# Kernel tuning notes

Hardware: AMD Instinct MI355X
Metric: run time of the kernel (lower is better)

## Reference

```python
import jax, jax.numpy as jnp
import numpy as np

HIDDEN = 1024
NUM_HEADS = 16
HEAD_DIM = HIDDEN // NUM_HEADS
EPS = 1e-12


def _layernorm(x, g, b):
    mu = jnp.mean(x, axis=-1, keepdims=True)
    var = jnp.var(x, axis=-1, keepdims=True)
    return (x - mu) * jax.lax.rsqrt(var + EPS) * g + b


def _attention(q, k, v, mask, Wd, bd, ln_g, ln_b):
    # q: [B,T,H], k/v: [B,S,H], mask: [B,1,1,S] additive
    B, T, _ = q.shape
    S = k.shape[1]
    qh = q.reshape(B, T, NUM_HEADS, HEAD_DIM).transpose(0, 2, 1, 3)  # [B,h,T,d]
    kh = k.reshape(B, S, NUM_HEADS, HEAD_DIM).transpose(0, 2, 1, 3)
    vh = v.reshape(B, S, NUM_HEADS, HEAD_DIM).transpose(0, 2, 1, 3)
    scores = jnp.einsum('bhtd,bhsd->bhts', qh, kh) / jnp.sqrt(jnp.float32(HEAD_DIM))
    if mask is not None:
        scores = scores + mask
    probs = jax.nn.softmax(scores, axis=-1)  # dropout = identity in eval
    ctx = jnp.einsum('bhts,bhsd->bthd', probs, vh)  # [B,T,h,d]
    # torch: w = dense.weight.t().view(h, d, H); einsum('bfnd,ndh->bfh')
    w = Wd.T.reshape(NUM_HEADS, HEAD_DIM, HIDDEN)
    proj = jnp.einsum('bthd,hdH->btH', ctx, w) + bd
    # residual is the (projected) query tensor q, per source
    return _layernorm(q + proj, ln_g, ln_b)


def setup_inputs() -> dict:
    key = jax.random.key(0)
    ks = jax.random.split(key, 12)
    s = 0.02
    B, S, T = 4, 1024, 1024
    return {
        'encoder_states': jax.random.normal(ks[0], (B, S, HIDDEN), jnp.float32),
        'decoder_inputs': jax.random.normal(ks[1], (B, T, HIDDEN), jnp.float32),
        'src_attention_mask': jnp.zeros((B, 1, 1, S), jnp.float32),
        'tgt_attention_mask': jnp.zeros((B, 1, 1, T), jnp.float32),
        'Wq': jax.random.normal(ks[2], (HIDDEN, HIDDEN), jnp.float32) * s,
        'bq': jnp.zeros((HIDDEN,), jnp.float32),
        'Wk': jax.random.normal(ks[3], (HIDDEN, HIDDEN), jnp.float32) * s,
        'bk': jnp.zeros((HIDDEN,), jnp.float32),
        'Wv': jax.random.normal(ks[4], (HIDDEN, HIDDEN), jnp.float32) * s,
        'bv': jnp.zeros((HIDDEN,), jnp.float32),
        'Wd': jax.random.normal(ks[5], (HIDDEN, HIDDEN), jnp.float32) * s,
        'bd': jnp.zeros((HIDDEN,), jnp.float32),
        'ln_g': jnp.ones((HIDDEN,), jnp.float32),
        'ln_b': jnp.zeros((HIDDEN,), jnp.float32),
    }


def reference(encoder_states, decoder_inputs, src_attention_mask, tgt_attention_mask,
              Wq, bq, Wk, bk, Wv, bv, Wd, bd, ln_g, ln_b):
    # projections (torch Linear: x @ W.T + b)
    q1 = decoder_inputs @ Wq.T + bq
    k1 = decoder_inputs @ Wk.T + bk
    v1 = decoder_inputs @ Wv.T + bv
    ek = encoder_states @ Wk.T + bk
    ev = encoder_states @ Wv.T + bv
    # self-attention over decoder states
    self_out = _attention(q1, k1, v1, tgt_attention_mask, Wd, bd, ln_g, ln_b)
    # cross-attention: query = self_out directly (no extra projection, per source)
    out = _attention(self_out, ek, ev, src_attention_mask, Wd, bd, ln_g, ln_b)
    return out
```

## Files before the change

kernel.cpp:

```cpp
#include <hip/hip_runtime.h>
#include <stdint.h>


#define B_   4
#define T_   1024
#define S_   1024
#define H_   1024
#define LOG2E 1.44269504088896340736f
#define SCALE_K (0.125f * LOG2E)

typedef __attribute__((ext_vector_type(8)))  __bf16       bf16x8;
typedef __attribute__((ext_vector_type(4)))  float        f32x4;
typedef __attribute__((ext_vector_type(16))) float        f32x16;
typedef __attribute__((ext_vector_type(4)))  unsigned int uint4v;

static __device__ __forceinline__ float bf2f(unsigned int u) {
    return __builtin_bit_cast(float, u << 16);
}
static __device__ __forceinline__ unsigned short f2bf(float f) {
    unsigned int x = __builtin_bit_cast(unsigned int, f);
    return (unsigned short)((x + 0x7fffu + ((x >> 16) & 1u)) >> 16);
}
static __device__ __forceinline__ unsigned int cvt_pk_bf16(float lo, float hi) {
    unsigned int r;
    asm("v_cvt_pk_bf16_f32 %0, %1, %2" : "=v"(r) : "v"(lo), "v"(hi));
    return r;
}
static __device__ __forceinline__ void perm32swap(unsigned int& a, unsigned int& b) {
    asm("v_permlane32_swap_b32 %0, %1" : "+v"(a), "+v"(b));
}
static __device__ __forceinline__ f32x4 mfma16(bf16x8 a, bf16x8 b, f32x4 c) {
    return __builtin_amdgcn_mfma_f32_16x16x32_bf16(a, b, c, 0, 0, 0);
}
static __device__ __forceinline__ f32x16 mfma32(bf16x8 a, bf16x8 b, f32x16 c) {
    return __builtin_amdgcn_mfma_f32_32x32x16_bf16(a, b, c, 0, 0, 0);
}

typedef const __attribute__((address_space(1))) void gv_t;
typedef __attribute__((address_space(3))) void lv_t;
static __device__ __forceinline__ void g2lds16(const void* g, void* l) {
    __builtin_amdgcn_global_load_lds((gv_t*)(size_t)g, (lv_t*)(unsigned int)(size_t)l, 16, 0, 0);
}

struct CvtArgs {
    const float* src[6];
    unsigned short* dst[6];
    float scale[6];
    int n4[6];
};
__global__ __launch_bounds__(256)
void cvt_multi(CvtArgs a) {
    const int k = blockIdx.y;
    const int i = blockIdx.x * 256 + threadIdx.x;
    if (i >= a.n4[k]) return;
    const float s = a.scale[k];
    float4 v = ((const float4*)a.src[k])[i];
    uint2 o;
    o.x = (unsigned)f2bf(v.x * s) | ((unsigned)f2bf(v.y * s) << 16);
    o.y = (unsigned)f2bf(v.z * s) | ((unsigned)f2bf(v.w * s) << 16);
    ((uint2*)a.dst[k])[i] = o;
}

struct GemmJob {
    const unsigned short* A[5];
    const unsigned short* W[5];
    const float* bias[5];
    float bs[5];
    unsigned short* O[5];
    unsigned short* OT[5];
    int koff[5];
    int klen[5];
};
__global__ __launch_bounds__(256, 4)
void gemm_bf16(GemmJob job)
{
    __shared__ char smem[32768];
    char* As = smem;
    char* Bs = smem + 16384;
    const int tid = threadIdx.x;
    const int lane = tid & 63;
    const int w = tid >> 6;
    const int c = lane & 15, g = lane >> 4;
    const int wm = (w >> 1) * 64, wn = (w & 1) * 64;
    const int m0 = blockIdx.x * 128;
    const int set = blockIdx.y >> 3;
    const int n0 = (blockIdx.y & 7) * 128;
    const unsigned short* A    = job.A[set];
    const unsigned short* W    = job.W[set];
    const float* bias          = job.bias[set];
    const float bscale         = job.bs[set];
    unsigned short* O          = job.O[set];
    unsigned short* OT         = job.OT[set];
    const int koff             = job.koff[set];
    const int kend             = koff + job.klen[set];

    f32x4 acc[4][4];
#pragma unroll
    for (int i = 0; i < 4; i++)
#pragma unroll
        for (int j = 0; j < 4; j++) acc[i][j] = (f32x4){0.f, 0.f, 0.f, 0.f};

    const int srow = w * 32 + (lane >> 3);
    const int swzc = ((lane & 7) ^ (lane >> 3)) * 8;
    const unsigned short* gA = A + (size_t)(m0 + srow) * 1024 + swzc;
    const unsigned short* gB = W + (size_t)(n0 + srow) * 1024 + swzc;
    char* lA = As + w * 4096;
    char* lB = Bs + w * 4096;

    for (int kk = koff; kk < kend; kk += 64) {
#pragma unroll
        for (int q = 0; q < 4; q++) {
            g2lds16(gA + kk + q*8192, lA + q*1024);
            g2lds16(gB + kk + q*8192, lB + q*1024);
        }
        __syncthreads();
#pragma unroll
        for (int ksub = 0; ksub < 2; ksub++) {
            bf16x8 af[4], bfr[4];
#pragma unroll
            for (int t = 0; t < 4; t++) {
                const int ra = wm + t*16 + c;
                const int rb = wn + t*16 + c;
                const int so = ((ksub*4 + g) ^ (c & 7)) << 4;
                af[t]  = *(const bf16x8*)(As + ra*128 + so);
                bfr[t] = *(const bf16x8*)(Bs + rb*128 + so);
            }
#pragma unroll
            for (int i = 0; i < 4; i++)
#pragma unroll
                for (int j = 0; j < 4; j++)
                    acc[i][j] = mfma16(af[i], bfr[j], acc[i][j]);
        }
        __syncthreads();
    }

    float bvv[4];
#pragma unroll
    for (int j = 0; j < 4; j++) bvv[j] = bias[n0 + wn + j*16 + c] * bscale;

    if (OT == nullptr) {
        char* eb = smem + w * 4096;
#pragma unroll
        for (int p = 0; p < 2; p++) {
#pragma unroll
            for (int ii = 0; ii < 2; ii++) {
                const int i = p*2 + ii;
#pragma unroll
                for (int j = 0; j < 4; j++)
#pragma unroll
                    for (int r = 0; r < 4; r++)
                        *(unsigned short*)(eb + (ii*16 + g*4 + r)*128 + (c + j*16)*2)
                            = f2bf(acc[i][j][r] + bvv[j]);
            }
            asm volatile("s_waitcnt lgkmcnt(0)" ::: "memory");
#pragma unroll
            for (int it = 0; it < 4; it++) {
                const int lrow = it*8 + (lane >> 3);
                uint4 vv = *(const uint4*)(eb + lrow*128 + (lane & 7)*16);
                *(uint4*)(O + (size_t)(m0 + wm + p*32 + lrow)*1024 + n0 + wn + (lane & 7)*8) = vv;
            }
            if (p == 0) asm volatile("s_waitcnt lgkmcnt(0)" ::: "memory");
        }
    } else {
        char* ebT = smem + w * 8192;
        const int n_glob = n0 + wn + lane;
        const int hh = n_glob >> 6, dd = n_glob & 63;
        const int bidx = m0 >> 10;
        unsigned short* vout0 = OT + ((size_t)((bidx*16 + hh)*64 + dd))*S_ + (m0 & 1023) + wm;
#pragma unroll
        for (int p = 0; p < 2; p++) {
#pragma unroll
            for (int ii = 0; ii < 2; ii++) {
                const int i = p*2 + ii;
#pragma unroll
                for (int j = 0; j < 4; j++) {
                    uint2 pw;
                    pw.x = (unsigned)f2bf(acc[i][j][0] + bvv[j]) |
                           ((unsigned)f2bf(acc[i][j][1] + bvv[j]) << 16);
                    pw.y = (unsigned)f2bf(acc[i][j][2] + bvv[j]) |
                           ((unsigned)f2bf(acc[i][j][3] + bvv[j]) << 16);
                    *(uint2*)(ebT + (j*16 + c)*72 + (ii*16 + g*4)*2) = pw;
                }
            }
            asm volatile("s_waitcnt lgkmcnt(0)" ::: "memory");
            unsigned short* vout = vout0 + p*32;
#pragma unroll
            for (int q = 0; q < 4; q++) {
                uint2 r0 = *(const uint2*)(ebT + lane*72 + (q*2    )*8);
                uint2 r1 = *(const uint2*)(ebT + lane*72 + (q*2 + 1)*8);
                uint4 vv; vv.x = r0.x; vv.y = r0.y; vv.z = r1.x; vv.w = r1.y;
                *(uint4*)(vout + q*8) = vv;
            }
            if (p == 0) asm volatile("s_waitcnt lgkmcnt(0)" ::: "memory");
        }
    }
}

__global__ __launch_bounds__(256, 4)
void attn_fused2(const unsigned short* __restrict__ Q,
                 const unsigned short* __restrict__ Kx,
                 const unsigned short* __restrict__ VT,
                 const float* __restrict__ mask,
                 unsigned short* __restrict__ Octx)
{
    __shared__ char smem[32768 + 4096 + 512 + 16];
    float* mb   = (float*)(smem + 32768);
    float* lbuf = (float*)(smem + 32768 + 4096);
    int* flag   = (int*)(smem + 32768 + 4096 + 512);

    const int tid = threadIdx.x;
    const int lane = tid & 63, w = tid >> 6;
    const int qc = lane & 31, hi = lane >> 5;
    const int bh = blockIdx.x, b = bh >> 4, h = bh & 15;
    const int q0 = blockIdx.y * 128 + w * 32;

    const int r0 = tid >> 3, sg = tid & 7;
    const unsigned short* gK0 = Kx + (size_t)(b*S_ + r0)*H_  + h*64 + sg*8;
    const unsigned short* gK1 = gK0 + (size_t)32*H_;
    const unsigned short* gV0 = VT + (size_t)(bh*64 + r0)*S_ + sg*8;
    const unsigned short* gV1 = gV0 + (size_t)32*S_;
    const int woff = r0*128 + ((sg*16) ^ ((r0 & 7) << 4));

    const unsigned short* qptr = Q + (size_t)(b*T_ + q0 + qc)*H_ + h*64 + hi*8;
    bf16x8 qf[4];
#pragma unroll
    for (int s = 0; s < 4; s++) qf[s] = *(const bf16x8*)(qptr + s*16);

    uint4 cK0 = *(const uint4*)gK0;
    uint4 cK1 = *(const uint4*)gK1;
    uint4 cV0 = *(const uint4*)gV0;
    uint4 cV1 = *(const uint4*)gV1;

    if (tid == 0) *flag = 0;
    __syncthreads();
    {
        float4 mv = ((const float4*)(mask + (size_t)b*S_))[tid];
        float4 ms;
        ms.x = mv.x * LOG2E; ms.y = mv.y * LOG2E; ms.z = mv.z * LOG2E; ms.w = mv.w * LOG2E;
        ((float4*)mb)[tid] = ms;
        if (mv.x != 0.f || mv.y != 0.f || mv.z != 0.f || mv.w != 0.f) atomicOr(flag, 1);
    }
    {
        char* b0 = smem;
        *(uint4*)(b0 + woff)               = cK0;
        *(uint4*)(b0 + 4096 + woff)        = cK1;
        *(uint4*)(b0 + 8192 + woff)        = cV0;
        *(uint4*)(b0 + 8192 + 4096 + woff) = cV1;
    }
    __syncthreads();
    const int msk = *flag;

    f32x16 o0 = {}, o1 = {};
    float lacc = 0.f;

    for (int t = 0; t < 16; ++t) {
        uint4 nK0, nK1, nV0, nV1;
        if (t < 15) {
            const size_t ko = (size_t)(t + 1) * 64 * H_;
            const int    vo = (t + 1) * 64;
            nK0 = *(const uint4*)(gK0 + ko);
            nK1 = *(const uint4*)(gK1 + ko);
            nV0 = *(const uint4*)(gV0 + vo);
            nV1 = *(const uint4*)(gV1 + vo);
        }
        char* Ks = smem + (t & 1) * 16384;
        char* Vs = Ks + 8192;

#pragma unroll
        for (int ts = 0; ts < 2; ++ts) {
            f32x16 st = {};
            __builtin_amdgcn_s_setprio(1);
#pragma unroll
            for (int step = 0; step < 4; ++step) {
                bf16x8 ak = *(const bf16x8*)(Ks + (ts*32 + qc)*128 +
                             ((step*32 + hi*16) ^ ((qc & 7) << 4)));
                st = mfma32(ak, qf[step], st);
            }
            __builtin_amdgcn_s_setprio(0);

            float pv[16];
            if (msk) {
#pragma unroll
                for (int rq = 0; rq < 4; ++rq) {
                    const float4 bb = *(const float4*)(mb + t*64 + ts*32 + rq*8 + hi*4);
#pragma unroll
                    for (int e = 0; e < 4; ++e)
                        pv[rq*4 + e] = __builtin_amdgcn_exp2f(st[rq*4 + e] + (&bb.x)[e]);
                }
            } else {
#pragma unroll
                for (int r = 0; r < 16; ++r) pv[r] = __builtin_amdgcn_exp2f(st[r]);
            }
#pragma unroll
            for (int r = 0; r < 16; ++r) lacc += pv[r];

#pragma unroll
            for (int half = 0; half < 2; ++half) {
                unsigned w0 = cvt_pk_bf16(pv[half*8 + 0], pv[half*8 + 1]);
                unsigned w1 = cvt_pk_bf16(pv[half*8 + 2], pv[half*8 + 3]);
                unsigned w2 = cvt_pk_bf16(pv[half*8 + 4], pv[half*8 + 5]);
                unsigned w3 = cvt_pk_bf16(pv[half*8 + 6], pv[half*8 + 7]);
                perm32swap(w0, w2);
                perm32swap(w1, w3);
                uint4v fw; fw[0] = w0; fw[1] = w1; fw[2] = w2; fw[3] = w3;
                const bf16x8 pa = __builtin_bit_cast(bf16x8, fw);
                const int scol = (ts*64 + half*32 + hi*16) ^ ((qc & 7) << 4);
                bf16x8 v0 = *(const bf16x8*)(Vs + qc*128        + scol);
                bf16x8 v1 = *(const bf16x8*)(Vs + (32 + qc)*128 + scol);
                __builtin_amdgcn_s_setprio(1);
                o0 = mfma32(pa, v0, o0);
                o1 = mfma32(pa, v1, o1);
                __builtin_amdgcn_s_setprio(0);
            }
        }

        if (t < 15) {
            char* nxt = smem + ((t + 1) & 1) * 16384;
            *(uint4*)(nxt + woff)               = nK0;
            *(uint4*)(nxt + 4096 + woff)        = nK1;
            *(uint4*)(nxt + 8192 + woff)        = nV0;
            *(uint4*)(nxt + 8192 + 4096 + woff) = nV1;
        }
        __syncthreads();
    }

    {
        unsigned la = __builtin_bit_cast(unsigned, lacc);
        unsigned lb = la;
        perm32swap(la, lb);
        const float ltot = __builtin_bit_cast(float, la) + __builtin_bit_cast(float, lb);
        const float linv = 1.f / ltot;
        if (hi == 0) lbuf[w*32 + qc] = linv;
    }
    __syncthreads();
    float4 li[4];
#pragma unroll
    for (int rq = 0; rq < 4; ++rq)
        li[rq] = *(const float4*)(lbuf + w*32 + rq*8 + hi*4);

#pragma unroll
    for (int dt = 0; dt < 2; ++dt) {
        const f32x16& oo = dt ? o1 : o0;
#pragma unroll
        for (int r = 0; r < 16; ++r) {
            const int qrow = (r & 3) + 8*(r >> 2) + 4*hi;
            const float val = oo[r] * (&li[r >> 2].x)[r & 3];
            Octx[(size_t)(b*T_ + q0 + qrow)*H_ + h*64 + dt*32 + qc] = f2bf(val);
        }
    }
}

template<int OUTMODE>
__global__ __launch_bounds__(256)
void ln_kernel(const unsigned short* __restrict__ resid,
               const unsigned short* __restrict__ projA,
               const unsigned short* __restrict__ projB,
               const float* __restrict__ gam,
               const float* __restrict__ bet,
               unsigned short* __restrict__ obf,
               float* __restrict__ of32)
{
    __shared__ float red[8];
    const int tid = threadIdx.x;
    const int lane = tid & 63, w = tid >> 6;
    const int i = tid * 4;
    const size_t base = (size_t)blockIdx.x * 1024 + i;
    uint2 rv = *(const uint2*)(resid + base);
    uint2 pv = *(const uint2*)(projA + base);
    uint2 qv = *(const uint2*)(projB + base);
    float x[4];
    x[0] = bf2f(rv.x & 0xffffu) + bf2f(pv.x & 0xffffu) + bf2f(qv.x & 0xffffu);
    x[1] = bf2f(rv.x >> 16)     + bf2f(pv.x >> 16)     + bf2f(qv.x >> 16);
    x[2] = bf2f(rv.y & 0xffffu) + bf2f(pv.y & 0xffffu) + bf2f(qv.y & 0xffffu);
    x[3] = bf2f(rv.y >> 16)     + bf2f(pv.y >> 16)     + bf2f(qv.y >> 16);
    float s = x[0] + x[1] + x[2] + x[3];
    float q = x[0]*x[0] + x[1]*x[1] + x[2]*x[2] + x[3]*x[3];
#pragma unroll
    for (int off = 1; off < 64; off <<= 1) {
        s += __shfl_xor(s, off);
        q += __shfl_xor(q, off);
    }
    if (lane == 0) { red[w*2] = s; red[w*2 + 1] = q; }
    __syncthreads();
    s = red[0] + red[2] + red[4] + red[6];
    q = red[1] + red[3] + red[5] + red[7];
    const float mu   = s * (1.f/1024.f);
    const float var  = q * (1.f/1024.f) - mu*mu;
    const float rstd = rsqrtf(var + 1e-12f);
    const float4 gv = *(const float4*)(gam + i);
    const float4 bv = *(const float4*)(bet + i);
    float y[4];
#pragma unroll
    for (int j = 0; j < 4; j++)
        y[j] = (x[j] - mu) * rstd * (&gv.x)[j] + (&bv.x)[j];
    if (OUTMODE == 0) {
        uint2 oo;
        oo.x = (unsigned)f2bf(y[0]) | ((unsigned)f2bf(y[1]) << 16);
        oo.y = (unsigned)f2bf(y[2]) | ((unsigned)f2bf(y[3]) << 16);
        *(uint2*)(obf + base) = oo;
    } else {
        float4 oo; oo.x = y[0]; oo.y = y[1]; oo.z = y[2]; oo.w = y[3];
        *(float4*)(of32 + base) = oo;
    }
}

extern "C" void kernel_launch(void* const* d_in, const int* in_sizes, int n_in,
                              void* d_out, int out_size, void* d_ws, size_t ws_size,
                              hipStream_t stream)
{
    const float* enc   = (const float*)d_in[0];
    const float* dec   = (const float*)d_in[1];
    const float* smask = (const float*)d_in[2];
    const float* tmask = (const float*)d_in[3];
    const float* Wq = (const float*)d_in[4];
    const float* bq = (const float*)d_in[5];
    const float* Wk = (const float*)d_in[6];
    const float* bk = (const float*)d_in[7];
    const float* Wv = (const float*)d_in[8];
    const float* bv = (const float*)d_in[9];
    const float* Wd = (const float*)d_in[10];
    const float* bd = (const float*)d_in[11];
    const float* lng = (const float*)d_in[12];
    const float* lnb = (const float*)d_in[13];
    float* out = (float*)d_out;

    char* ws = (char*)d_ws;
    const size_t MB = 1024ull * 1024ull;
    unsigned short* dec_bf = (unsigned short*)(ws + 0*MB);
    unsigned short* enc_bf = (unsigned short*)(ws + 8*MB);
    unsigned short* Wq_bf  = (unsigned short*)(ws + 16*MB);
    unsigned short* Wk_bf  = (unsigned short*)(ws + 18*MB);
    unsigned short* Wv_bf  = (unsigned short*)(ws + 20*MB);
    unsigned short* Wd_bf  = (unsigned short*)(ws + 22*MB);
    unsigned short* q1  = (unsigned short*)(ws + 24*MB);
    unsigned short* k1  = (unsigned short*)(ws + 32*MB);
    unsigned short* vt1 = (unsigned short*)(ws + 40*MB);
    unsigned short* ek  = (unsigned short*)(ws + 48*MB);
    unsigned short* evt = (unsigned short*)(ws + 56*MB);
    unsigned short* ctx      = dec_bf;
    unsigned short* proj     = enc_bf;
    unsigned short* projb    = vt1;
    unsigned short* self_out = k1;

    CvtArgs ca;
    ca.src[0] = dec; ca.dst[0] = dec_bf; ca.scale[0] = 1.f;      ca.n4[0] = 1048576;
    ca.src[1] = enc; ca.dst[1] = enc_bf; ca.scale[1] = 1.f;      ca.n4[1] = 1048576;
    ca.src[2] = Wq;  ca.dst[2] = Wq_bf;  ca.scale[2] = 1.f;      ca.n4[2] = 262144;
    ca.src[3] = Wk;  ca.dst[3] = Wk_bf;  ca.scale[3] = SCALE_K;  ca.n4[3] = 262144;
    ca.src[4] = Wv;  ca.dst[4] = Wv_bf;  ca.scale[4] = 1.f;      ca.n4[4] = 262144;
    ca.src[5] = Wd;  ca.dst[5] = Wd_bf;  ca.scale[5] = 1.f;      ca.n4[5] = 262144;
    cvt_multi<<<dim3(4096, 6), 256, 0, stream>>>(ca);

    GemmJob j1;
    j1.A[0] = dec_bf; j1.W[0] = Wq_bf; j1.bias[0] = bq; j1.bs[0] = 1.f;     j1.O[0] = q1; j1.OT[0] = nullptr;
    j1.A[1] = dec_bf; j1.W[1] = Wk_bf; j1.bias[1] = bk; j1.bs[1] = SCALE_K; j1.O[1] = k1; j1.OT[1] = nullptr;
    j1.A[2] = dec_bf; j1.W[2] = Wv_bf; j1.bias[2] = bv; j1.bs[2] = 1.f;     j1.O[2] = nullptr; j1.OT[2] = vt1;
    j1.A[3] = enc_bf; j1.W[3] = Wk_bf; j1.bias[3] = bk; j1.bs[3] = SCALE_K; j1.O[3] = ek; j1.OT[3] = nullptr;
    j1.A[4] = enc_bf; j1.W[4] = Wv_bf; j1.bias[4] = bv; j1.bs[4] = 1.f;     j1.O[4] = nullptr; j1.OT[4] = evt;
    for (int i = 0; i < 5; i++) { j1.koff[i] = 0; j1.klen[i] = 1024; }
    gemm_bf16<<<dim3(32, 40), 256, 0, stream>>>(j1);

    GemmJob jd;
    for (int i = 0; i < 5; i++) {
        jd.A[i] = ctx; jd.W[i] = Wd_bf; jd.bias[i] = bd; jd.bs[i] = 1.f;
        jd.O[i] = proj; jd.OT[i] = nullptr; jd.koff[i] = 0; jd.klen[i] = 512;
    }
    jd.bs[1] = 0.f; jd.O[1] = projb; jd.koff[1] = 512;

    attn_fused2<<<dim3(64, 8), 256, 0, stream>>>(q1, k1, vt1, tmask, ctx);
    gemm_bf16<<<dim3(32, 16), 256, 0, stream>>>(jd);
    ln_kernel<0><<<4096, 256, 0, stream>>>(q1, proj, projb, lng, lnb, self_out, nullptr);

    attn_fused2<<<dim3(64, 8), 256, 0, stream>>>(self_out, ek, evt, smask, ctx);
    gemm_bf16<<<dim3(32, 16), 256, 0, stream>>>(jd);
    ln_kernel<1><<<4096, 256, 0, stream>>>(self_out, proj, projb, lng, lnb, nullptr, out);
}
```

Measured before the change: 158.5 us.

## Split attention key range across two wave groups and reduce partial outputs in LDS

The attention kernel now launches 512 threads per block. Two groups of four waves each process half of the 1024 keys with their own double-buffered LDS region, and the partial outputs and row sums are combined through shared memory before normalisation and store. This doubles the waves per block to hide latency and halves the serial loop length. The cost is twice the LDS per block, an extra reduction and barrier, and possibly fewer resident blocks. The GEMM launch-bound occupancy hint is also lowered from 4 to 2, which can give the compiler more registers per thread.

New measurement: 165.2 us. 4.2% more time.

```diff
diff --git a/kernel.cpp b/kernel.cpp
--- a/kernel.cpp
+++ b/kernel.cpp
@@ -71,7 +71,7 @@
     int koff[5];
     int klen[5];
 };
-__global__ __launch_bounds__(256, 4)
+__global__ __launch_bounds__(256, 2)
 void gemm_bf16(GemmJob job)
 {
     __shared__ char smem[32768];
@@ -196,30 +196,33 @@
     }
 }
 
-__global__ __launch_bounds__(256, 4)
-void attn_fused2(const unsigned short* __restrict__ Q,
+__global__ __launch_bounds__(512, 4)
+void attn_fused5(const unsigned short* __restrict__ Q,
                  const unsigned short* __restrict__ Kx,
                  const unsigned short* __restrict__ VT,
                  const float* __restrict__ mask,
                  unsigned short* __restrict__ Octx)
 {
-    __shared__ char smem[32768 + 4096 + 512 + 16];
-    float* mb   = (float*)(smem + 32768);
-    float* lbuf = (float*)(smem + 32768 + 4096);
-    int* flag   = (int*)(smem + 32768 + 4096 + 512);
+    __shared__ char smem[65536 + 4096 + 512 + 16];
+    float* mb   = (float*)(smem + 65536);
+    float* lbuf = (float*)(smem + 65536 + 4096);
+    int* flag   = (int*)(smem + 65536 + 4096 + 512);
 
     const int tid = threadIdx.x;
     const int lane = tid & 63, w = tid >> 6;
+    const int wg = w & 3, shalf = w >> 2;
     const int qc = lane & 31, hi = lane >> 5;
     const int bh = blockIdx.x, b = bh >> 4, h = bh & 15;
-    const int q0 = blockIdx.y * 128 + w * 32;
-
-    const int r0 = tid >> 3, sg = tid & 7;
-    const unsigned short* gK0 = Kx + (size_t)(b*S_ + r0)*H_  + h*64 + sg*8;
+    const int q0 = blockIdx.y * 128 + wg * 32;
+
+    const int tg = tid & 255;
+    const int rs = tg >> 3, sg = tg & 7;
+    const unsigned short* gK0 = Kx + (size_t)(b*S_ + shalf*512 + rs)*H_ + h*64 + sg*8;
     const unsigned short* gK1 = gK0 + (size_t)32*H_;
-    const unsigned short* gV0 = VT + (size_t)(bh*64 + r0)*S_ + sg*8;
+    const unsigned short* gV0 = VT + (size_t)(bh*64 + rs)*S_ + shalf*512 + sg*8;
     const unsigned short* gV1 = gV0 + (size_t)32*S_;
-    const int woff = r0*128 + ((sg*16) ^ ((r0 & 7) << 4));
+    const int woff = rs*128 + ((sg*16) ^ ((rs & 7) << 4));
+    char* sbase = smem + shalf * 32768;
 
     const unsigned short* qptr = Q + (size_t)(b*T_ + q0 + qc)*H_ + h*64 + hi*8;
     bf16x8 qf[4];
@@ -233,7 +236,7 @@
 
     if (tid == 0) *flag = 0;
     __syncthreads();
-    {
+    if (tid < 256) {
         float4 mv = ((const float4*)(mask + (size_t)b*S_))[tid];
         float4 ms;
         ms.x = mv.x * LOG2E; ms.y = mv.y * LOG2E; ms.z = mv.z * LOG2E; ms.w = mv.w * LOG2E;
@@ -241,11 +244,11 @@
         if (mv.x != 0.f || mv.y != 0.f || mv.z != 0.f || mv.w != 0.f) atomicOr(flag, 1);
     }
     {
-        char* b0 = smem;
-        *(uint4*)(b0 + woff)               = cK0;
-        *(uint4*)(b0 + 4096 + woff)        = cK1;
-        *(uint4*)(b0 + 8192 + woff)        = cV0;
-        *(uint4*)(b0 + 8192 + 4096 + woff) = cV1;
+        char* b0 = sbase;
+        *(uint4*)(b0 + woff)                = cK0;
+        *(uint4*)(b0 + 4096 + woff)         = cK1;
+        *(uint4*)(b0 + 8192 + woff)         = cV0;
+        *(uint4*)(b0 + 8192 + 4096 + woff)  = cV1;
     }
     __syncthreads();
     const int msk = *flag;
@@ -253,9 +256,9 @@
     f32x16 o0 = {}, o1 = {};
     float lacc = 0.f;
 
-    for (int t = 0; t < 16; ++t) {
+    for (int t = 0; t < 8; ++t) {
         uint4 nK0, nK1, nV0, nV1;
-        if (t < 15) {
+        if (t < 7) {
             const size_t ko = (size_t)(t + 1) * 64 * H_;
             const int    vo = (t + 1) * 64;
             nK0 = *(const uint4*)(gK0 + ko);
@@ -263,8 +266,8 @@
             nV0 = *(const uint4*)(gV0 + vo);
             nV1 = *(const uint4*)(gV1 + vo);
         }
-        char* Ks = smem + (t & 1) * 16384;
-        char* Vs = Ks + 8192;
+        const char* Ks = sbase + (t & 1) * 16384;
+        const char* Vs = Ks + 8192;
 
 #pragma unroll
         for (int ts = 0; ts < 2; ++ts) {
@@ -282,7 +285,7 @@
             if (msk) {
 #pragma unroll
                 for (int rq = 0; rq < 4; ++rq) {
-                    const float4 bb = *(const float4*)(mb + t*64 + ts*32 + rq*8 + hi*4);
+                    const float4 bb = *(const float4*)(mb + shalf*512 + t*64 + ts*32 + rq*8 + hi*4);
 #pragma unroll
                     for (int e = 0; e < 4; ++e)
                         pv[rq*4 + e] = __builtin_amdgcn_exp2f(st[rq*4 + e] + (&bb.x)[e]);
@@ -314,8 +317,8 @@
             }
         }
 
-        if (t < 15) {
-            char* nxt = smem + ((t + 1) & 1) * 16384;
+        if (t < 7) {
+            char* nxt = sbase + ((t + 1) & 1) * 16384;
             *(uint4*)(nxt + woff)               = nK0;
             *(uint4*)(nxt + 4096 + woff)        = nK1;
             *(uint4*)(nxt + 8192 + woff)        = nV0;
@@ -324,28 +327,44 @@
         __syncthreads();
     }
 
-    {
+    float* slot = (float*)smem + (wg*64 + lane)*34;
+    if (shalf == 1) {
+#pragma unroll
+        for (int r = 0; r < 16; ++r) {
+            slot[r]      = o0[r];
+            slot[16 + r] = o1[r];
+        }
+        slot[32] = lacc;
+    }
+    __syncthreads();
+    if (shalf == 0) {
+#pragma unroll
+        for (int r = 0; r < 16; ++r) {
+            o0[r] += slot[r];
+            o1[r] += slot[16 + r];
+        }
+        lacc += slot[32];
         unsigned la = __builtin_bit_cast(unsigned, lacc);
         unsigned lb = la;
         perm32swap(la, lb);
         const float ltot = __builtin_bit_cast(float, la) + __builtin_bit_cast(float, lb);
-        const float linv = 1.f / ltot;
-        if (hi == 0) lbuf[w*32 + qc] = linv;
+        if (hi == 0) lbuf[wg*32 + qc] = 1.f / ltot;
     }
     __syncthreads();
-    float4 li[4];
-#pragma unroll
-    for (int rq = 0; rq < 4; ++rq)
-        li[rq] = *(const float4*)(lbuf + w*32 + rq*8 + hi*4);
-
-#pragma unroll
-    for (int dt = 0; dt < 2; ++dt) {
-        const f32x16& oo = dt ? o1 : o0;
-#pragma unroll
-        for (int r = 0; r < 16; ++r) {
-            const int qrow = (r & 3) + 8*(r >> 2) + 4*hi;
-            const float val = oo[r] * (&li[r >> 2].x)[r & 3];
-            Octx[(size_t)(b*T_ + q0 + qrow)*H_ + h*64 + dt*32 + qc] = f2bf(val);
+    if (shalf == 0) {
+        float4 li[4];
+#pragma unroll
+        for (int rq = 0; rq < 4; ++rq)
+            li[rq] = *(const float4*)(lbuf + wg*32 + rq*8 + hi*4);
+#pragma unroll
+        for (int dt = 0; dt < 2; ++dt) {
+            const f32x16& oo = dt ? o1 : o0;
+#pragma unroll
+            for (int r = 0; r < 16; ++r) {
+                const int qrow = (r & 3) + 8*(r >> 2) + 4*hi;
+                const float val = oo[r] * (&li[r >> 2].x)[r & 3];
+                Octx[(size_t)(b*T_ + q0 + qrow)*H_ + h*64 + dt*32 + qc] = f2bf(val);
+            }
         }
     }
 }
@@ -467,11 +486,11 @@
     }
     jd.bs[1] = 0.f; jd.O[1] = projb; jd.koff[1] = 512;
 
-    attn_fused2<<<dim3(64, 8), 256, 0, stream>>>(q1, k1, vt1, tmask, ctx);
+    attn_fused5<<<dim3(64, 8), 512, 0, stream>>>(q1, k1, vt1, tmask, ctx);
     gemm_bf16<<<dim3(32, 16), 256, 0, stream>>>(jd);
     ln_kernel<0><<<4096, 256, 0, stream>>>(q1, proj, projb, lng, lnb, self_out, nullptr);
 
-    attn_fused2<<<dim3(64, 8), 256, 0, stream>>>(self_out, ek, evt, smask, ctx);
+    attn_fused5<<<dim3(64, 8), 512, 0, stream>>>(self_out, ek, evt, smask, ctx);
     gemm_bf16<<<dim3(32, 16), 256, 0, stream>>>(jd);
     ln_kernel<1><<<4096, 256, 0, stream>>>(self_out, proj, projb, lng, lnb, nullptr, out);
 }
```
